# Optimization experiments

Measured on AMD Instinct MI355X. Metric: run time of the kernel, lower is better.

## Reference

```python
import jax, jax.numpy as jnp
import numpy as np

NUM_HEAD = 16
HIDDEN = 1024
HEAD_DIM = HIDDEN // NUM_HEAD


def setup_inputs() -> dict:
    key = jax.random.key(0)
    k1, k2, k3, k4, k5 = jax.random.split(key, 5)
    scale = 0.02
    x = jax.random.normal(k1, (2, 2048, HIDDEN), dtype=jnp.float32)
    w_in = jax.random.normal(k2, (3 * HIDDEN, HIDDEN), dtype=jnp.float32) * scale
    b_in = jax.random.normal(k3, (3 * HIDDEN,), dtype=jnp.float32) * scale
    w_out = jax.random.normal(k4, (HIDDEN, HIDDEN), dtype=jnp.float32) * scale
    b_out = jax.random.normal(k5, (HIDDEN,), dtype=jnp.float32) * scale
    return {"x": x, "w_in": w_in, "b_in": b_in, "w_out": w_out, "b_out": b_out}


def reference(x, w_in, b_in, w_out, b_out):
    B, S, D = x.shape
    # in_proj: fused QKV, torch Linear convention y = x @ W.T + b
    qkv = x @ w_in.T + b_in                      # [B,S,3D]
    q, k, v = jnp.split(qkv, 3, axis=-1)         # each [B,S,D]
    def heads(t):
        return t.reshape(B, S, NUM_HEAD, HEAD_DIM).transpose(0, 2, 1, 3)  # [B,H,S,d]
    q, k, v = heads(q), heads(k), heads(v)
    scores = jnp.einsum("bhqd,bhkd->bhqk", q, k) / jnp.sqrt(
        jnp.asarray(HEAD_DIM, dtype=x.dtype))    # [B,H,S,S]
    attn = jax.nn.softmax(scores, axis=-1)
    out = jnp.einsum("bhqk,bhkd->bhqd", attn, v)  # [B,H,S,d]
    out = out.transpose(0, 2, 1, 3).reshape(B, S, D)
    return out @ w_out.T + b_out
```

## Files before the change

### kernel.cpp

```cpp
#include <hip/hip_runtime.h>

using u16 = unsigned short;
using u32 = unsigned int;

typedef __bf16 bf16x8 __attribute__((ext_vector_type(8)));
typedef __bf16 bf16x2 __attribute__((ext_vector_type(2)));
typedef float f32x4 __attribute__((ext_vector_type(4)));

__device__ __forceinline__ u16 f2b(float x) {
  u32 u = __builtin_bit_cast(u32, x);
  u += 0x7fffu + ((u >> 16) & 1u);
  return (u16)(u >> 16);
}

__device__ __forceinline__ u32 pk2(float lo, float hi) {
  bf16x2 t;
  t[0] = (__bf16)lo;
  t[1] = (__bf16)hi;
  return __builtin_bit_cast(u32, t);
}

__device__ __forceinline__ void gload16(const u16* g, u16* l) {
  __builtin_amdgcn_global_load_lds(
      (const __attribute__((address_space(1))) void*)g,
      (__attribute__((address_space(3))) void*)l, 16, 0, 0);
}

#define SCALE_Q 0.1803368801111204f

__global__ void cvt_bf16_k(const float* __restrict__ s, u16* __restrict__ d, int n8) {
  int i = blockIdx.x * blockDim.x + threadIdx.x;
  int stride = gridDim.x * blockDim.x;
  for (; i < n8; i += stride) {
    float4 a = ((const float4*)s)[2 * i];
    float4 b = ((const float4*)s)[2 * i + 1];
    uint4 o;
    o.x = (u32)f2b(a.x) | ((u32)f2b(a.y) << 16);
    o.y = (u32)f2b(a.z) | ((u32)f2b(a.w) << 16);
    o.z = (u32)f2b(b.x) | ((u32)f2b(b.y) << 16);
    o.w = (u32)f2b(b.z) | ((u32)f2b(b.w) << 16);
    ((uint4*)d)[i] = o;
  }
}

template <int MODE, int BM>
__global__ __launch_bounds__(256) void gemm_bt(
    const u16* __restrict__ A, const u16* __restrict__ Bm,
    const float* __restrict__ bias,
    u16* __restrict__ q, u16* __restrict__ k, u16* __restrict__ v,
    float* __restrict__ outf) {
  constexpr int KD = 1024;
  constexpr int MR = BM / 32;
  const int n0 = blockIdx.x * 128;
  const int m0 = blockIdx.y * BM;
  const int tid = threadIdx.x;
  const int wid = tid >> 6;
  const int lane = tid & 63;
  const int wr = wid >> 1, wc = wid & 1;
  const int fr = lane & 15, fg = lane >> 4;
  const int srow = lane >> 2;
  const int scol = (lane & 3) * 8;

  __shared__ __align__(16) u16 As[BM * 32];
  __shared__ __align__(16) u16 Bs[128 * 32];

  f32x4 acc[MR][4] = {};

  for (int k0 = 0; k0 < KD; k0 += 32) {
#pragma unroll
    for (int i = 0; i < BM / 64; ++i) {
      int row = i * 64 + wid * 16 + srow;
      gload16(A + (size_t)(m0 + row) * KD + k0 + scol, As + (i * 64 + wid * 16) * 32);
    }
#pragma unroll
    for (int i = 0; i < 2; ++i) {
      int row = i * 64 + wid * 16 + srow;
      gload16(Bm + (size_t)(n0 + row) * KD + k0 + scol, Bs + (i * 64 + wid * 16) * 32);
    }
    __syncthreads();
    bf16x8 af[MR], bfr[4];
#pragma unroll
    for (int r = 0; r < MR; ++r)
      af[r] = *(const bf16x8*)(As + (wr * (BM / 2) + r * 16 + fr) * 32 + fg * 8);
#pragma unroll
    for (int c = 0; c < 4; ++c)
      bfr[c] = *(const bf16x8*)(Bs + (wc * 64 + c * 16 + fr) * 32 + fg * 8);
#pragma unroll
    for (int r = 0; r < MR; ++r)
#pragma unroll
      for (int c = 0; c < 4; ++c)
        acc[r][c] = __builtin_amdgcn_mfma_f32_16x16x32_bf16(af[r], bfr[c], acc[r][c], 0, 0, 0);
    __syncthreads();
  }

#pragma unroll
  for (int r = 0; r < MR; ++r) {
#pragma unroll
    for (int c = 0; c < 4; ++c) {
      const int gcol = n0 + wc * 64 + c * 16 + fr;
      const float bv = bias[gcol];
#pragma unroll
      for (int g = 0; g < 4; ++g) {
        const int grow = m0 + wr * (BM / 2) + r * 16 + fg * 4 + g;
        float val = acc[r][c][g] + bv;
        if (MODE == 0) {
          const int which = gcol >> 10;
          if (which == 0) val *= SCALE_Q;
          const int dcol = gcol & 1023;
          const int hh = dcol >> 6, dd = dcol & 63;
          const int bb = grow >> 11, ss = grow & 2047;
          u16* dst = which == 0 ? q : (which == 1 ? k : v);
          dst[((size_t)((bb << 4) + hh) * 2048 + ss) * 64 + dd] = f2b(val);
        } else {
          outf[(size_t)grow * 1024 + gcol] = val;
        }
      }
    }
  }
}

__global__ __launch_bounds__(256) void attn_fwd(
    const u16* __restrict__ Q, const u16* __restrict__ K,
    const u16* __restrict__ V, u16* __restrict__ AO) {
  const int wg = blockIdx.x;
  const int newid = (wg & 7) * 64 + (wg >> 3);
  const int bh = newid >> 4;
  const int qt = newid & 15;
  const int b = bh >> 4, h = bh & 15;

  const int tid = threadIdx.x, wid = tid >> 6, lane = tid & 63;
  const int fr = lane & 15, fg = lane >> 4;
  const size_t base = (size_t)bh * (2048 * 64);
  const int q0 = qt * 128 + wid * 32;

  constexpr int LD = 72;
  __shared__ __align__(16) u16 Ks[2][64 * LD];
  __shared__ __align__(16) u16 Vs[2][64 * LD];

  bf16x8 qf[2][2];
#pragma unroll
  for (int rf = 0; rf < 2; ++rf)
#pragma unroll
    for (int ks = 0; ks < 2; ++ks)
      qf[rf][ks] = *(const bf16x8*)(Q + base + (size_t)(q0 + rf * 16 + fr) * 64 + ks * 32 + fg * 8);

  f32x4 o[2][4] = {};
  float mrow[2] = {-3.0e38f, -3.0e38f};
  float lrow[2] = {0.f, 0.f};

  const int krow = lane;
  const int Lrow = ((krow >> 5) << 5) | (((krow >> 3) & 1) << 4) | (((krow >> 2) & 1) << 3) |
                   (((krow >> 4) & 1) << 2) | (krow & 3);
  const int c0 = wid * 16;

  uint4 kr0, kr1, vr0, vr1;
  {
    const u16* kp = K + base + (size_t)Lrow * 64 + c0;
    const u16* vp = V + base + (size_t)krow * 64 + c0;
    kr0 = *(const uint4*)kp; kr1 = *(const uint4*)(kp + 8);
    vr0 = *(const uint4*)vp; vr1 = *(const uint4*)(vp + 8);
  }

  for (int t = 0; t < 32; ++t) {
    u16* kb = (u16*)Ks[t & 1];
    u16* vb = (u16*)Vs[t & 1];
    *(uint4*)(kb + krow * LD + c0) = kr0;
    *(uint4*)(kb + krow * LD + c0 + 8) = kr1;
    {
      u32 vv[8] = {vr0.x, vr0.y, vr0.z, vr0.w, vr1.x, vr1.y, vr1.z, vr1.w};
#pragma unroll
      for (int j = 0; j < 8; ++j) {
        vb[(c0 + 2 * j) * LD + krow]     = (u16)(vv[j] & 0xffffu);
        vb[(c0 + 2 * j + 1) * LD + krow] = (u16)(vv[j] >> 16);
      }
    }
    __syncthreads();
    if (t + 1 < 32) {
      const u16* kp = K + base + (size_t)((t + 1) * 64 + Lrow) * 64 + c0;
      const u16* vp = V + base + (size_t)((t + 1) * 64 + krow) * 64 + c0;
      kr0 = *(const uint4*)kp; kr1 = *(const uint4*)(kp + 8);
      vr0 = *(const uint4*)vp; vr1 = *(const uint4*)(vp + 8);
    }

    bf16x8 kf[4][2], vf[4][2];
#pragma unroll
    for (int c = 0; c < 4; ++c)
#pragma unroll
      for (int ks = 0; ks < 2; ++ks)
        kf[c][ks] = *(const bf16x8*)(kb + (c * 16 + fr) * LD + ks * 32 + fg * 8);
#pragma unroll
    for (int d = 0; d < 4; ++d)
#pragma unroll
      for (int ks = 0; ks < 2; ++ks)
        vf[d][ks] = *(const bf16x8*)(vb + (d * 16 + fr) * LD + ks * 32 + fg * 8);

#pragma unroll
    for (int rf = 0; rf < 2; ++rf) {
      f32x4 p[4];
#pragma unroll
      for (int c = 0; c < 4; ++c) {
        f32x4 z = {};
        z = __builtin_amdgcn_mfma_f32_16x16x32_bf16(kf[c][0], qf[rf][0], z, 0, 0, 0);
        z = __builtin_amdgcn_mfma_f32_16x16x32_bf16(kf[c][1], qf[rf][1], z, 0, 0, 0);
        p[c] = z;
      }
      f32x4 m4 = p[0];
#pragma unroll
      for (int c = 1; c < 4; ++c) {
        m4[0] = fmaxf(m4[0], p[c][0]); m4[1] = fmaxf(m4[1], p[c][1]);
        m4[2] = fmaxf(m4[2], p[c][2]); m4[3] = fmaxf(m4[3], p[c][3]);
      }
      float mx = fmaxf(fmaxf(m4[0], m4[1]), fmaxf(m4[2], m4[3]));
      mx = fmaxf(mx, __shfl_xor(mx, 16));
      mx = fmaxf(mx, __shfl_xor(mx, 32));
      const float mold = mrow[rf];
      const float mnew = fmaxf(mold, mx);
      const float corr = exp2f(mold - mnew);
      mrow[rf] = mnew;
      float rs = 0.f;
#pragma unroll
      for (int c = 0; c < 4; ++c)
#pragma unroll
        for (int g = 0; g < 4; ++g) {
          const float pv = exp2f(p[c][g] - mnew);
          p[c][g] = pv;
          rs += pv;
        }
      rs += __shfl_xor(rs, 16);
      rs += __shfl_xor(rs, 32);
      lrow[rf] = lrow[rf] * corr + rs;

      bf16x8 pa[2];
#pragma unroll
      for (int ks = 0; ks < 2; ++ks) {
        u32 w0 = pk2(p[2 * ks][0], p[2 * ks][1]);
        u32 w1 = pk2(p[2 * ks][2], p[2 * ks][3]);
        u32 w2 = pk2(p[2 * ks + 1][0], p[2 * ks + 1][1]);
        u32 w3 = pk2(p[2 * ks + 1][2], p[2 * ks + 1][3]);
        uint4 packed = {w0, w1, w2, w3};
        pa[ks] = __builtin_bit_cast(bf16x8, packed);
      }

      float cO[4];
#pragma unroll
      for (int g = 0; g < 4; ++g) cO[g] = __shfl(corr, 20 * fg + g);
#pragma unroll
      for (int d = 0; d < 4; ++d) {
        o[rf][d][0] *= cO[0]; o[rf][d][1] *= cO[1];
        o[rf][d][2] *= cO[2]; o[rf][d][3] *= cO[3];
      }
#pragma unroll
      for (int d = 0; d < 4; ++d) {
        o[rf][d] = __builtin_amdgcn_mfma_f32_16x16x32_bf16(pa[0], vf[d][0], o[rf][d], 0, 0, 0);
        o[rf][d] = __builtin_amdgcn_mfma_f32_16x16x32_bf16(pa[1], vf[d][1], o[rf][d], 0, 0, 0);
      }
    }
  }

#pragma unroll
  for (int rf = 0; rf < 2; ++rf) {
    float lO[4], rinv[4];
#pragma unroll
    for (int g = 0; g < 4; ++g) lO[g] = __shfl(lrow[rf], 20 * fg + g);
#pragma unroll
    for (int g = 0; g < 4; ++g) rinv[g] = 1.0f / lO[g];
#pragma unroll
    for (int d = 0; d < 4; ++d)
#pragma unroll
      for (int g = 0; g < 4; ++g) {
        const int qr = q0 + rf * 16 + fg * 4 + g;
        AO[(size_t)(b * 2048 + qr) * 1024 + h * 64 + d * 16 + fr] = f2b(o[rf][d][g] * rinv[g]);
      }
  }
}

extern "C" void kernel_launch(void* const* d_in, const int* in_sizes, int n_in,
                              void* d_out, int out_size, void* d_ws, size_t ws_size,
                              hipStream_t stream) {
  (void)in_sizes; (void)n_in; (void)out_size; (void)ws_size;
  const float* x     = (const float*)d_in[0];
  const float* w_in  = (const float*)d_in[1];
  const float* b_in  = (const float*)d_in[2];
  const float* w_out = (const float*)d_in[3];
  const float* b_out = (const float*)d_in[4];

  u16* xb    = (u16*)d_ws;
  u16* winb  = xb    + (size_t)4096 * 1024;
  u16* woutb = winb  + (size_t)3072 * 1024;
  u16* qb    = woutb + (size_t)1024 * 1024;
  u16* kb    = qb    + (size_t)4194304;
  u16* vb    = kb    + (size_t)4194304;
  u16* aob   = vb    + (size_t)4194304;

  cvt_bf16_k<<<2048, 256, 0, stream>>>(x, xb, 4096 * 1024 / 8);
  cvt_bf16_k<<<1536, 256, 0, stream>>>(w_in, winb, 3072 * 1024 / 8);
  cvt_bf16_k<<<512, 256, 0, stream>>>(w_out, woutb, 1024 * 1024 / 8);

  gemm_bt<0, 128><<<dim3(24, 32), 256, 0, stream>>>(xb, winb, b_in, qb, kb, vb, nullptr);
  attn_fwd<<<512, 256, 0, stream>>>(qb, kb, vb, aob);
  gemm_bt<1, 64><<<dim3(8, 64), 256, 0, stream>>>(aob, woutb, b_out, nullptr, nullptr, nullptr,
                                                  (float*)d_out);
}
```

Baseline: 222.0 us.

## Defer softmax rescaling, pack V transpose stores, add MFMA priority hints

```diff
diff --git a/kernel.cpp b/kernel.cpp
--- a/kernel.cpp
+++ b/kernel.cpp
@@ -27,6 +27,7 @@
 }
 
 #define SCALE_Q 0.1803368801111204f
+#define DEFER_THR 8.0f
 
 __global__ void cvt_bf16_k(const float* __restrict__ s, u16* __restrict__ d, int n8) {
   int i = blockIdx.x * blockDim.x + threadIdx.x;
@@ -152,13 +153,15 @@
   const int Lrow = ((krow >> 5) << 5) | (((krow >> 3) & 1) << 4) | (((krow >> 2) & 1) << 3) |
                    (((krow >> 4) & 1) << 2) | (krow & 3);
   const int c0 = wid * 16;
+  const int kp2 = (lane & 31) * 2;
+  const int vh = (lane >> 5) * 8;
 
   uint4 kr0, kr1, vr0, vr1;
   {
     const u16* kp = K + base + (size_t)Lrow * 64 + c0;
-    const u16* vp = V + base + (size_t)krow * 64 + c0;
+    const u16* vp = V + base + (size_t)kp2 * 64 + c0 + vh;
     kr0 = *(const uint4*)kp; kr1 = *(const uint4*)(kp + 8);
-    vr0 = *(const uint4*)vp; vr1 = *(const uint4*)(vp + 8);
+    vr0 = *(const uint4*)vp; vr1 = *(const uint4*)(vp + 64);
   }
 
   for (int t = 0; t < 32; ++t) {
@@ -167,19 +170,21 @@
     *(uint4*)(kb + krow * LD + c0) = kr0;
     *(uint4*)(kb + krow * LD + c0 + 8) = kr1;
     {
-      u32 vv[8] = {vr0.x, vr0.y, vr0.z, vr0.w, vr1.x, vr1.y, vr1.z, vr1.w};
+      const u32* ra = (const u32*)&vr0;
+      const u32* rb = (const u32*)&vr1;
 #pragma unroll
       for (int j = 0; j < 8; ++j) {
-        vb[(c0 + 2 * j) * LD + krow]     = (u16)(vv[j] & 0xffffu);
-        vb[(c0 + 2 * j + 1) * LD + krow] = (u16)(vv[j] >> 16);
+        u32 w = __builtin_amdgcn_perm(rb[j >> 1], ra[j >> 1],
+                                      (j & 1) ? 0x07060302u : 0x05040100u);
+        *(u32*)(vb + (c0 + vh + j) * LD + kp2) = w;
       }
     }
     __syncthreads();
     if (t + 1 < 32) {
       const u16* kp = K + base + (size_t)((t + 1) * 64 + Lrow) * 64 + c0;
-      const u16* vp = V + base + (size_t)((t + 1) * 64 + krow) * 64 + c0;
+      const u16* vp = V + base + (size_t)((t + 1) * 64 + kp2) * 64 + c0 + vh;
       kr0 = *(const uint4*)kp; kr1 = *(const uint4*)(kp + 8);
-      vr0 = *(const uint4*)vp; vr1 = *(const uint4*)(vp + 8);
+      vr0 = *(const uint4*)vp; vr1 = *(const uint4*)(vp + 64);
     }
 
     bf16x8 kf[4][2], vf[4][2];
@@ -197,6 +202,7 @@
 #pragma unroll
     for (int rf = 0; rf < 2; ++rf) {
       f32x4 p[4];
+      __builtin_amdgcn_s_setprio(1);
 #pragma unroll
       for (int c = 0; c < 4; ++c) {
         f32x4 z = {};
@@ -204,6 +210,7 @@
         z = __builtin_amdgcn_mfma_f32_16x16x32_bf16(kf[c][1], qf[rf][1], z, 0, 0, 0);
         p[c] = z;
       }
+      __builtin_amdgcn_s_setprio(0);
       f32x4 m4 = p[0];
 #pragma unroll
       for (int c = 1; c < 4; ++c) {
@@ -213,22 +220,39 @@
       float mx = fmaxf(fmaxf(m4[0], m4[1]), fmaxf(m4[2], m4[3]));
       mx = fmaxf(mx, __shfl_xor(mx, 16));
       mx = fmaxf(mx, __shfl_xor(mx, 32));
+
       const float mold = mrow[rf];
-      const float mnew = fmaxf(mold, mx);
-      const float corr = exp2f(mold - mnew);
-      mrow[rf] = mnew;
+      const bool defer = __all(mx <= mold + DEFER_THR);
+      float mnew = mold, corr = 1.0f;
+      if (!defer) {
+        mnew = fmaxf(mold, mx);
+        corr = __builtin_amdgcn_exp2f(mold - mnew);
+        mrow[rf] = mnew;
+      }
       float rs = 0.f;
 #pragma unroll
       for (int c = 0; c < 4; ++c)
 #pragma unroll
         for (int g = 0; g < 4; ++g) {
-          const float pv = exp2f(p[c][g] - mnew);
+          const float pv = __builtin_amdgcn_exp2f(p[c][g] - mnew);
           p[c][g] = pv;
           rs += pv;
         }
       rs += __shfl_xor(rs, 16);
       rs += __shfl_xor(rs, 32);
-      lrow[rf] = lrow[rf] * corr + rs;
+      if (defer) {
+        lrow[rf] += rs;
+      } else {
+        lrow[rf] = lrow[rf] * corr + rs;
+        float cO[4];
+#pragma unroll
+        for (int g = 0; g < 4; ++g) cO[g] = __shfl(corr, 20 * fg + g);
+#pragma unroll
+        for (int d = 0; d < 4; ++d) {
+          o[rf][d][0] *= cO[0]; o[rf][d][1] *= cO[1];
+          o[rf][d][2] *= cO[2]; o[rf][d][3] *= cO[3];
+        }
+      }
 
       bf16x8 pa[2];
 #pragma unroll
@@ -240,30 +264,22 @@
         uint4 packed = {w0, w1, w2, w3};
         pa[ks] = __builtin_bit_cast(bf16x8, packed);
       }
-
-      float cO[4];
-#pragma unroll
-      for (int g = 0; g < 4; ++g) cO[g] = __shfl(corr, 20 * fg + g);
-#pragma unroll
-      for (int d = 0; d < 4; ++d) {
-        o[rf][d][0] *= cO[0]; o[rf][d][1] *= cO[1];
-        o[rf][d][2] *= cO[2]; o[rf][d][3] *= cO[3];
-      }
+      __builtin_amdgcn_s_setprio(1);
 #pragma unroll
       for (int d = 0; d < 4; ++d) {
         o[rf][d] = __builtin_amdgcn_mfma_f32_16x16x32_bf16(pa[0], vf[d][0], o[rf][d], 0, 0, 0);
         o[rf][d] = __builtin_amdgcn_mfma_f32_16x16x32_bf16(pa[1], vf[d][1], o[rf][d], 0, 0, 0);
       }
+      __builtin_amdgcn_s_setprio(0);
     }
   }
 
 #pragma unroll
   for (int rf = 0; rf < 2; ++rf) {
-    float lO[4], rinv[4];
-#pragma unroll
-    for (int g = 0; g < 4; ++g) lO[g] = __shfl(lrow[rf], 20 * fg + g);
-#pragma unroll
-    for (int g = 0; g < 4; ++g) rinv[g] = 1.0f / lO[g];
+    float rinv[4];
+#pragma unroll
+    for (int g = 0; g < 4; ++g)
+      rinv[g] = __builtin_amdgcn_rcpf(__shfl(lrow[rf], 20 * fg + g));
 #pragma unroll
     for (int d = 0; d < 4; ++d)
 #pragma unroll
```

Result: faster. 199.0 us (-10.3%).
